# Optimization experiments

Hardware: AMD Instinct MI355X
Metric: run time of the kernel (lower is better)

Reference implementation:

```python
import jax, jax.numpy as jnp
import numpy as np

B, L, S, D, H = 4, 1024, 1024, 1024, 16
HD = D // H  # head_dim = 64


def setup_inputs() -> dict:
    key = jax.random.key(0)
    ks = jax.random.split(key, 12)
    s = 1.0 / np.sqrt(D)
    return {
        "query": jax.random.normal(ks[0], (B, L, D), jnp.float32),
        "key": jax.random.normal(ks[1], (B, S, D), jnp.float32),
        "value": jax.random.normal(ks[2], (B, S, D), jnp.float32),
        "key_padding_mask": jax.random.randint(ks[3], (B, S), 0, 2) > 0,
        "Wq": jax.random.normal(ks[4], (D, D), jnp.float32) * s,
        "bq": jnp.zeros((D,), jnp.float32),
        "Wk": jax.random.normal(ks[5], (D, D), jnp.float32) * s,
        "bk": jnp.zeros((D,), jnp.float32),
        "Wv": jax.random.normal(ks[6], (D, D), jnp.float32) * s,
        "bv": jnp.zeros((D,), jnp.float32),
        "Wo": jax.random.normal(ks[7], (D, D), jnp.float32) * s,
        "bo": jnp.zeros((D,), jnp.float32),
    }


def reference(query, key, value, key_padding_mask, Wq, bq, Wk, bk, Wv, bv, Wo, bo):
    bs, tgt, _ = query.shape
    src = key.shape[1]
    # Q/K/V projections (nn.Linear: x @ W.T + b)
    q = query @ Wq.T + bq
    k = key @ Wk.T + bk
    v = value @ Wv.T + bv
    # split heads: (B, T, H, HD)
    q = q.reshape(bs, tgt, H, HD)
    k = k.reshape(bs, src, H, HD)
    v = v.reshape(bs, src, H, HD)
    # scaled dot-product attention with key padding mask (True = masked)
    scale = 1.0 / jnp.sqrt(jnp.asarray(HD, q.dtype))
    scores = jnp.einsum("blhd,bshd->bhls", q, k) * scale  # (B,H,L,S)
    neg_inf = jnp.asarray(-jnp.inf, scores.dtype)
    scores = scores + jnp.where(key_padding_mask[:, None, None, :], neg_inf, 0.0)
    attn = jax.nn.softmax(scores, axis=-1)
    out = jnp.einsum("bhls,bshd->blhd", attn, v).reshape(bs, tgt, D)
    return out @ Wo.T + bo
```

## Files before the change

kernel.cpp:

```cpp
#include <hip/hip_runtime.h>
#include <hip/hip_bf16.h>


typedef __bf16 bf16;
typedef __bf16 bf16x8 __attribute__((ext_vector_type(8)));
typedef float floatx4 __attribute__((ext_vector_type(4)));

#define D_MODEL 1024
#define NHEAD   16
#define HDIM    64
#define BATCH   4
#define SEQ     1024
#define M_ROWS  (BATCH * SEQ)
#define ACT_N   ((size_t)M_ROWS * D_MODEL)
#define W_N     ((size_t)D_MODEL * D_MODEL)
#define SC2     0.18033688011112042f

#define GLD(gp, lp) __builtin_amdgcn_global_load_lds( \
    (__attribute__((address_space(1))) void*)(gp), \
    (__attribute__((address_space(3))) void*)(lp), 16, 0, 0)

__global__ __launch_bounds__(256)
void k_convert_all(const float* __restrict__ a0, const float* __restrict__ a1,
                   const float* __restrict__ a2,
                   const float* __restrict__ w0, const float* __restrict__ w1,
                   const float* __restrict__ w2, const float* __restrict__ w3,
                   bf16* __restrict__ dst,
                   const unsigned* __restrict__ m, float* __restrict__ mbias)
{
    if (blockIdx.x == 8192) {
        __shared__ unsigned viol[4];
        __shared__ int fmsh;
        if (threadIdx.x < 4) viol[threadIdx.x] = 0;
        __syncthreads();
        unsigned a = 0, b = 0, c = 0, d = 0;
        for (int i = threadIdx.x; i < 1024; i += 256) {
            unsigned v = m[i];
            if (v > 1u) a = 1;
            if (((v & 0xFFu) > 1u) || (((v >> 8) & 0xFFu) > 1u) ||
                (((v >> 16) & 0xFFu) > 1u) || (((v >> 24) & 0xFFu) > 1u)) b = 1;
            unsigned lo = v & 0xFFFFu, hi = v >> 16;
            if (!((lo == 0u || lo == 0x3F80u) && (hi == 0u || hi == 0x3F80u))) c = 1;
            if (lo != 0u) d = 1;
        }
        if (a) atomicOr(&viol[0], 1u);
        if (b) atomicOr(&viol[1], 1u);
        if (c) atomicOr(&viol[2], 1u);
        if (d) atomicOr(&viol[3], 1u);
        __syncthreads();
        if (threadIdx.x == 0) {
            int fm;
            if (!viol[0])      fm = 1;
            else if (!viol[1]) fm = 0;
            else if (!viol[2]) fm = viol[3] ? 2 : 3;
            else               fm = 0;
            fmsh = fm;
        }
        __syncthreads();
        const int fm = fmsh;
        for (int i = 0; i < 16; ++i) {
            int s = i * 256 + threadIdx.x;
            bool msk;
            if (fm == 1)      msk = ((const int*)m)[s] != 0;
            else if (fm == 2) msk = ((const unsigned short*)m)[s] != 0;
            else if (fm == 3) msk = ((const unsigned*)m)[s] != 0;
            else              msk = ((const unsigned char*)m)[s] != 0;
            mbias[s] = msk ? -1e30f : 0.f;
        }
        return;
    }

    size_t i = ((size_t)blockIdx.x * 256 + threadIdx.x) * 8;
    const float* src; size_t off;
    if (i < ((size_t)12 << 20)) {
        int z = (int)(i >> 22);
        src = (z == 0) ? a0 : (z == 1) ? a1 : a2;
        off = i & (((size_t)1 << 22) - 1);
    } else {
        size_t r = i - ((size_t)12 << 20);
        int j = (int)(r >> 20);
        src = (j == 0) ? w0 : (j == 1) ? w1 : (j == 2) ? w2 : w3;
        off = r & (((size_t)1 << 20) - 1);
    }
    float4 f0 = ((const float4*)(src + off))[0];
    float4 f1 = ((const float4*)(src + off))[1];
    bf16x8 o;
    o[0] = (bf16)f0.x; o[1] = (bf16)f0.y; o[2] = (bf16)f0.z; o[3] = (bf16)f0.w;
    o[4] = (bf16)f1.x; o[5] = (bf16)f1.y; o[6] = (bf16)f1.z; o[7] = (bf16)f1.w;
    *(bf16x8*)(dst + i) = o;
}

template<typename CT>
__device__ __forceinline__ void gemm_core(const bf16* __restrict__ A,
                                          const bf16* __restrict__ W,
                                          const float* __restrict__ bias,
                                          CT* __restrict__ C,
                                          int m0, int n0, bool rowBias)
{
    __shared__ alignas(16) bf16 As[2][128 * 32];
    __shared__ alignas(16) bf16 Bs[2][128 * 32];

    const int t    = threadIdx.x;
    const int lane = t & 63;
    const int w    = t >> 6;
    const int wm   = w >> 1, wn = w & 1;
    const int l15  = lane & 15;
    const int quad = lane >> 4;

    floatx4 acc[4][4] = {};

    #pragma unroll
    for (int i = 0; i < 2; ++i) {
        int c   = i * 256 + t;
        int row = c >> 2;
        int ck  = ((c & 3) ^ ((row >> 1) & 3)) * 8;
        int lo  = (i * 256 + w * 64) * 8;
        GLD(A + (size_t)(m0 + row) * D_MODEL + ck, As[0] + lo);
        GLD(W + (size_t)(n0 + row) * D_MODEL + ck, Bs[0] + lo);
    }
    __syncthreads();

    int cur = 0;
    for (int k0 = 0; k0 < D_MODEL; k0 += 32) {
        if (k0 + 32 < D_MODEL) {
            #pragma unroll
            for (int i = 0; i < 2; ++i) {
                int c   = i * 256 + t;
                int row = c >> 2;
                int ck  = ((c & 3) ^ ((row >> 1) & 3)) * 8;
                int lo  = (i * 256 + w * 64) * 8;
                GLD(A + (size_t)(m0 + row) * D_MODEL + k0 + 32 + ck, As[cur ^ 1] + lo);
                GLD(W + (size_t)(n0 + row) * D_MODEL + k0 + 32 + ck, Bs[cur ^ 1] + lo);
            }
        }

        bf16x8 af[4], bfr[4];
        #pragma unroll
        for (int i = 0; i < 4; ++i) {
            int r = wm * 64 + i * 16 + l15;
            af[i] = *(const bf16x8*)&As[cur][r * 32 + (quad ^ ((r >> 1) & 3)) * 8];
        }
        #pragma unroll
        for (int j = 0; j < 4; ++j) {
            int r = wn * 64 + j * 16 + l15;
            bfr[j] = *(const bf16x8*)&Bs[cur][r * 32 + (quad ^ ((r >> 1) & 3)) * 8];
        }

        #pragma unroll
        for (int i = 0; i < 4; ++i)
            #pragma unroll
            for (int j = 0; j < 4; ++j)
                acc[i][j] = __builtin_amdgcn_mfma_f32_16x16x32_bf16(
                    af[i], bfr[j], acc[i][j], 0, 0, 0);

        __syncthreads();
        cur ^= 1;
    }

    #pragma unroll
    for (int i = 0; i < 4; ++i) {
        int rowb = m0 + wm * 64 + i * 16 + quad * 4;
        float bvr[4];
        if (rowBias) {
            #pragma unroll
            for (int r = 0; r < 4; ++r) bvr[r] = bias[rowb + r];
        }
        #pragma unroll
        for (int j = 0; j < 4; ++j) {
            int col = n0 + wn * 64 + j * 16 + l15;
            float bc = rowBias ? 0.f : bias[col];
            #pragma unroll
            for (int r = 0; r < 4; ++r) {
                float val = acc[i][j][r] + (rowBias ? bvr[r] : bc);
                C[(size_t)(rowb + r) * D_MODEL + col] = (CT)val;
            }
        }
    }
}

__global__ __launch_bounds__(256)
void k_gemm_proj(const bf16* __restrict__ cq, const bf16* __restrict__ ck,
                 const bf16* __restrict__ cv,
                 const bf16* __restrict__ cWq, const bf16* __restrict__ cWk,
                 const bf16* __restrict__ cWv,
                 const float* __restrict__ bq, const float* __restrict__ bk,
                 const float* __restrict__ bv,
                 bf16* __restrict__ qproj, bf16* __restrict__ kproj,
                 bf16* __restrict__ vt)
{
    const int bid = blockIdx.x;
    const int x = bid & 7;
    const int j = bid >> 3;
    const int p = x * 12 + (j >> 3);
    const int n0 = (j & 7) * 128;
    if (p < 64) {
        int z = p >> 5, m0 = (p & 31) * 128;
        gemm_core<bf16>(z ? ck : cq, z ? cWk : cWq, z ? bk : bq,
                        z ? kproj : qproj, m0, n0, false);
    } else {
        int pv = p - 64;
        int b = pv >> 3, m0 = (pv & 7) * 128;
        gemm_core<bf16>(cWv, cv + (size_t)b * W_N, bv,
                        vt + (size_t)b * W_N, m0, n0, true);
    }
}

__global__ __launch_bounds__(256)
void k_gemm_o(const bf16* __restrict__ A, const bf16* __restrict__ W,
              const float* __restrict__ bb, float* __restrict__ C)
{
    const int bid = blockIdx.x;
    const int x = bid & 7;
    const int j = bid >> 3;
    const int p = x * 4 + (j >> 3);
    const int n0 = (j & 7) * 128;
    gemm_core<float>(A, W, bb, C, p * 128, n0, false);
}

__global__ __launch_bounds__(256)
void k_attn(const bf16* __restrict__ qproj, const bf16* __restrict__ kproj,
            const bf16* __restrict__ vt, const float* __restrict__ mbias_g,
            bf16* __restrict__ ctx)
{
    __shared__ alignas(16) bf16 Kst[2][4096];
    __shared__ alignas(16) bf16 Vst[2][4096];
    __shared__ alignas(16) bf16 Past[4096];

    const int t    = threadIdx.x;
    const int lane = t & 63;
    const int w    = t >> 6;
    const int l15  = lane & 15;
    const int quad = lane >> 4;

    const int b  = blockIdx.x >> 4;
    const int h  = blockIdx.x & 15;
    const int q0 = blockIdx.y * 64;

    #pragma unroll
    for (int kk = 0; kk < 2; ++kk) {
        const bf16* gp = qproj + (size_t)(b * SEQ + q0 + w * 16 + l15) * D_MODEL
                       + h * HDIM + kk * 32 + quad * 8;
        GLD(gp, Past + (w * 2 + kk) * 512);
    }
    #pragma unroll
    for (int i = 0; i < 2; ++i) {
        int f   = w * 2 + i;
        int row = (f >> 1) * 16 + l15;
        int cb  = (f & 1) * 32 + quad * 8;
        GLD(kproj + (size_t)(b * SEQ + row) * D_MODEL + h * HDIM + cb,
            Kst[0] + f * 512);
        GLD(vt + (size_t)(b * 1024 + h * HDIM + row) * D_MODEL + cb,
            Vst[0] + f * 512);
    }
    __syncthreads();

    bf16x8 qf[2];
    #pragma unroll
    for (int kk = 0; kk < 2; ++kk)
        qf[kk] = *(const bf16x8*)&Past[(w * 2 + kk) * 512 + lane * 8];

    bf16x8 ones;
    #pragma unroll
    for (int e = 0; e < 8; ++e) ones[e] = (bf16)1.0f;

    floatx4 o[4] = {};
    floatx4 accl = {};

    const int pbase = w * 1024 + (l15 >> 3) * 128 + quad * 32 + (l15 & 7);
    const float* __restrict__ mbb = mbias_g + b * SEQ;

    int cur = 0;
    for (int s0 = 0; s0 < SEQ; s0 += 64) {
        if (s0 + 64 < SEQ) {
            #pragma unroll
            for (int i = 0; i < 2; ++i) {
                int f   = w * 2 + i;
                int row = (f >> 1) * 16 + l15;
                int cb  = (f & 1) * 32 + quad * 8;
                GLD(kproj + (size_t)(b * SEQ + s0 + 64 + row) * D_MODEL
                        + h * HDIM + cb,
                    Kst[cur ^ 1] + f * 512);
                GLD(vt + (size_t)(b * 1024 + h * HDIM + row) * D_MODEL
                        + s0 + 64 + cb,
                    Vst[cur ^ 1] + f * 512);
            }
        }

        floatx4 s_acc[4] = {};
        #pragma unroll
        for (int j = 0; j < 4; ++j)
            #pragma unroll
            for (int kk = 0; kk < 2; ++kk) {
                bf16x8 kf = *(const bf16x8*)&Kst[cur][(j * 2 + kk) * 512 + lane * 8];
                s_acc[j] = __builtin_amdgcn_mfma_f32_16x16x32_bf16(
                    qf[kk], kf, s_acc[j], 0, 0, 0);
            }

        #pragma unroll
        for (int j = 0; j < 4; ++j) {
            float mb = mbb[s0 + j * 16 + l15];
            #pragma unroll
            for (int r = 0; r < 4; ++r) {
                float p = __builtin_amdgcn_exp2f(fmaf(s_acc[j][r], SC2, mb));
                Past[pbase + (j >> 1) * 512 + (j & 1) * 256 + r * 8] = (bf16)p;
            }
        }
        __builtin_amdgcn_wave_barrier();

        bf16x8 pf[2];
        #pragma unroll
        for (int kk = 0; kk < 2; ++kk)
            pf[kk] = *(const bf16x8*)&Past[w * 1024 + kk * 512 + lane * 8];

        #pragma unroll
        for (int kk = 0; kk < 2; ++kk)
            accl = __builtin_amdgcn_mfma_f32_16x16x32_bf16(pf[kk], ones, accl,
                                                           0, 0, 0);
        #pragma unroll
        for (int j = 0; j < 4; ++j)
            #pragma unroll
            for (int kk = 0; kk < 2; ++kk) {
                bf16x8 vf = *(const bf16x8*)&Vst[cur][(j * 2 + kk) * 512 + lane * 8];
                o[j] = __builtin_amdgcn_mfma_f32_16x16x32_bf16(
                    pf[kk], vf, o[j], 0, 0, 0);
            }

        __syncthreads();
        cur ^= 1;
    }

    float inv[4];
    #pragma unroll
    for (int r = 0; r < 4; ++r) inv[r] = (accl[r] > 0.f) ? 1.f / accl[r] : 0.f;
    #pragma unroll
    for (int j = 0; j < 4; ++j)
        #pragma unroll
        for (int r = 0; r < 4; ++r) {
            int row = q0 + w * 16 + quad * 4 + r;
            int col = h * HDIM + j * 16 + l15;
            ctx[(size_t)(b * SEQ + row) * D_MODEL + col] = (bf16)(o[j][r] * inv[r]);
        }
}

extern "C" void kernel_launch(void* const* d_in, const int* in_sizes, int n_in,
                              void* d_out, int out_size, void* d_ws, size_t ws_size,
                              hipStream_t stream)
{
    char* wsb = (char*)d_ws;
    float* mbias = (float*)wsb;
    bf16* cbase = (bf16*)(wsb + 65536);
    bf16 *cq = cbase, *ck = cq + ACT_N, *cv = ck + ACT_N;
    bf16 *cWq = cv + ACT_N, *cWk = cWq + W_N, *cWv = cWk + W_N, *cWo = cWv + W_N;
    bf16* qproj = cWo + W_N;
    bf16* kproj = qproj + ACT_N;
    bf16* vt    = kproj + ACT_N;
    bf16* ctx   = vt + ACT_N;
    float* out  = (float*)d_out;

    k_convert_all<<<8193, 256, 0, stream>>>(
        (const float*)d_in[0], (const float*)d_in[1], (const float*)d_in[2],
        (const float*)d_in[4], (const float*)d_in[6], (const float*)d_in[8],
        (const float*)d_in[10], cbase, (const unsigned*)d_in[3], mbias);

    k_gemm_proj<<<768, 256, 0, stream>>>(cq, ck, cv, cWq, cWk, cWv,
                                         (const float*)d_in[5],
                                         (const float*)d_in[7],
                                         (const float*)d_in[9],
                                         qproj, kproj, vt);
    k_attn<<<dim3(64, 16), 256, 0, stream>>>(qproj, kproj, vt, mbias, ctx);
    k_gemm_o<<<256, 256, 0, stream>>>(ctx, cWo, (const float*)d_in[11], out);
}
```

Measured before the change: 236.5 us.

## Triple-buffer GEMM LDS tiles with two-deep prefetch and partial vmcnt waits

Moves the GEMM core from double to triple buffering in LDS, prefetching two K-tiles ahead with global_load_lds. The full __syncthreads after each step becomes an inline s_waitcnt vmcnt(4) plus s_barrier, so only the oldest tile's loads must land before the barrier. This aims to hide global memory latency behind MFMA work. In exchange LDS use grows by half, which may reduce occupancy, and the hand-written vmcnt counts rely on the compiler not emitting other outstanding vector memory ops.

```diff
diff --git a/kernel.cpp b/kernel.cpp
--- a/kernel.cpp
+++ b/kernel.cpp
@@ -90,6 +90,18 @@
     *(bf16x8*)(dst + i) = o;
 }
 
+#define STAGE_TILE(k0s, bsel) do {                                          \
+    _Pragma("unroll")                                                       \
+    for (int ii = 0; ii < 2; ++ii) {                                        \
+        int c   = ii * 256 + t;                                             \
+        int row = c >> 2;                                                   \
+        int ck  = ((c & 3) ^ ((row >> 1) & 3)) * 8;                         \
+        int lo  = (ii * 256 + w * 64) * 8;                                  \
+        GLD(A + (size_t)(m0 + row) * D_MODEL + (k0s) + ck, As[bsel] + lo);  \
+        GLD(W + (size_t)(n0 + row) * D_MODEL + (k0s) + ck, Bs[bsel] + lo);  \
+    }                                                                       \
+} while (0)
+
 template<typename CT>
 __device__ __forceinline__ void gemm_core(const bf16* __restrict__ A,
                                           const bf16* __restrict__ W,
@@ -97,8 +109,8 @@
                                           CT* __restrict__ C,
                                           int m0, int n0, bool rowBias)
 {
-    __shared__ alignas(16) bf16 As[2][128 * 32];
-    __shared__ alignas(16) bf16 Bs[2][128 * 32];
+    __shared__ alignas(16) bf16 As[3][128 * 32];
+    __shared__ alignas(16) bf16 Bs[3][128 * 32];
 
     const int t    = threadIdx.x;
     const int lane = t & 63;
@@ -109,29 +121,16 @@
 
     floatx4 acc[4][4] = {};
 
-    #pragma unroll
-    for (int i = 0; i < 2; ++i) {
-        int c   = i * 256 + t;
-        int row = c >> 2;
-        int ck  = ((c & 3) ^ ((row >> 1) & 3)) * 8;
-        int lo  = (i * 256 + w * 64) * 8;
-        GLD(A + (size_t)(m0 + row) * D_MODEL + ck, As[0] + lo);
-        GLD(W + (size_t)(n0 + row) * D_MODEL + ck, Bs[0] + lo);
-    }
-    __syncthreads();
+    STAGE_TILE(0, 0);
+    STAGE_TILE(32, 1);
+    asm volatile("s_waitcnt vmcnt(4)\n\ts_barrier" ::: "memory");
 
     int cur = 0;
     for (int k0 = 0; k0 < D_MODEL; k0 += 32) {
-        if (k0 + 32 < D_MODEL) {
-            #pragma unroll
-            for (int i = 0; i < 2; ++i) {
-                int c   = i * 256 + t;
-                int row = c >> 2;
-                int ck  = ((c & 3) ^ ((row >> 1) & 3)) * 8;
-                int lo  = (i * 256 + w * 64) * 8;
-                GLD(A + (size_t)(m0 + row) * D_MODEL + k0 + 32 + ck, As[cur ^ 1] + lo);
-                GLD(W + (size_t)(n0 + row) * D_MODEL + k0 + 32 + ck, Bs[cur ^ 1] + lo);
-            }
+        const int pre = k0 + 64;
+        if (pre < D_MODEL) {
+            int nb = cur + 2; if (nb >= 3) nb -= 3;
+            STAGE_TILE(pre, nb);
         }
 
         bf16x8 af[4], bfr[4];
@@ -153,8 +152,12 @@
                 acc[i][j] = __builtin_amdgcn_mfma_f32_16x16x32_bf16(
                     af[i], bfr[j], acc[i][j], 0, 0, 0);
 
-        __syncthreads();
-        cur ^= 1;
+        if (pre < D_MODEL)
+            asm volatile("s_waitcnt vmcnt(4)\n\ts_barrier" ::: "memory");
+        else
+            asm volatile("s_waitcnt vmcnt(0)\n\ts_barrier" ::: "memory");
+
+        ++cur; if (cur == 3) cur = 0;
     }
 
     #pragma unroll
```

Result: no change. 240.8 us (+1.8%).

## Fuse fp32-to-bf16 activation conversion into projection GEMM tile loads

Applied to the files above, without the earlier changes.

The separate conversion of the query, key and value activations to bf16 is removed. The projection GEMM now loads fp32 tiles into registers, converts them, and writes bf16 into LDS after the MFMA step, overlapping the conversion with compute. This removes one full write and read of a 24 MB bf16 activation copy. The cost is that fp32 activations are read once per output column tile, which doubles the bytes per load, and the register-staged path replaces the direct global-to-LDS loads, adding register pressure and VALU conversion work inside the GEMM loop.

```diff
diff --git a/kernel.cpp b/kernel.cpp
--- a/kernel.cpp
+++ b/kernel.cpp
@@ -20,15 +20,21 @@
     (__attribute__((address_space(1))) void*)(gp), \
     (__attribute__((address_space(3))) void*)(lp), 16, 0, 0)
 
+__device__ __forceinline__ bf16x8 cvt8(const float4& f0, const float4& f1)
+{
+    bf16x8 o;
+    o[0] = (bf16)f0.x; o[1] = (bf16)f0.y; o[2] = (bf16)f0.z; o[3] = (bf16)f0.w;
+    o[4] = (bf16)f1.x; o[5] = (bf16)f1.y; o[6] = (bf16)f1.z; o[7] = (bf16)f1.w;
+    return o;
+}
+
 __global__ __launch_bounds__(256)
-void k_convert_all(const float* __restrict__ a0, const float* __restrict__ a1,
-                   const float* __restrict__ a2,
-                   const float* __restrict__ w0, const float* __restrict__ w1,
-                   const float* __restrict__ w2, const float* __restrict__ w3,
-                   bf16* __restrict__ dst,
-                   const unsigned* __restrict__ m, float* __restrict__ mbias)
-{
-    if (blockIdx.x == 8192) {
+void k_convert_w(const float* __restrict__ w0, const float* __restrict__ w1,
+                 const float* __restrict__ w2, const float* __restrict__ w3,
+                 bf16* __restrict__ dst,
+                 const unsigned* __restrict__ m, float* __restrict__ mbias)
+{
+    if (blockIdx.x == 2048) {
         __shared__ unsigned viol[4];
         __shared__ int fmsh;
         if (threadIdx.x < 4) viol[threadIdx.x] = 0;
@@ -71,28 +77,49 @@
     }
 
     size_t i = ((size_t)blockIdx.x * 256 + threadIdx.x) * 8;
-    const float* src; size_t off;
-    if (i < ((size_t)12 << 20)) {
-        int z = (int)(i >> 22);
-        src = (z == 0) ? a0 : (z == 1) ? a1 : a2;
-        off = i & (((size_t)1 << 22) - 1);
-    } else {
-        size_t r = i - ((size_t)12 << 20);
-        int j = (int)(r >> 20);
-        src = (j == 0) ? w0 : (j == 1) ? w1 : (j == 2) ? w2 : w3;
-        off = r & (((size_t)1 << 20) - 1);
-    }
+    int j = (int)(i >> 20);
+    const float* src = (j == 0) ? w0 : (j == 1) ? w1 : (j == 2) ? w2 : w3;
+    size_t off = i & (((size_t)1 << 20) - 1);
     float4 f0 = ((const float4*)(src + off))[0];
     float4 f1 = ((const float4*)(src + off))[1];
-    bf16x8 o;
-    o[0] = (bf16)f0.x; o[1] = (bf16)f0.y; o[2] = (bf16)f0.z; o[3] = (bf16)f0.w;
-    o[4] = (bf16)f1.x; o[5] = (bf16)f1.y; o[6] = (bf16)f1.z; o[7] = (bf16)f1.w;
-    *(bf16x8*)(dst + i) = o;
-}
-
-template<typename CT>
-__device__ __forceinline__ void gemm_core(const bf16* __restrict__ A,
-                                          const bf16* __restrict__ W,
+    *(bf16x8*)(dst + i) = cvt8(f0, f1);
+}
+
+template<bool F32>
+__device__ __forceinline__ void stage_issue(const void* __restrict__ base,
+                                            int r0, int kk,
+                                            const int srow[2], const int schk[2],
+                                            const int sx[2], int w,
+                                            bf16* lds, float4 pre[2][2])
+{
+    #pragma unroll
+    for (int ii = 0; ii < 2; ++ii) {
+        if constexpr (F32) {
+            const float* g = (const float*)base
+                + (size_t)(r0 + srow[ii]) * D_MODEL + kk + schk[ii] * 8;
+            pre[ii][0] = ((const float4*)g)[0];
+            pre[ii][1] = ((const float4*)g)[1];
+        } else {
+            GLD((const bf16*)base + (size_t)(r0 + srow[ii]) * D_MODEL + kk + sx[ii] * 8,
+                lds + (ii * 256 + w * 64) * 8);
+        }
+    }
+}
+
+template<bool F32>
+__device__ __forceinline__ void stage_write(const int srow[2], const int sx[2],
+                                            bf16* lds, const float4 pre[2][2])
+{
+    if constexpr (F32) {
+        #pragma unroll
+        for (int ii = 0; ii < 2; ++ii)
+            *(bf16x8*)&lds[srow[ii] * 32 + sx[ii] * 8] = cvt8(pre[ii][0], pre[ii][1]);
+    }
+}
+
+template<typename CT, bool AF32, bool WF32>
+__device__ __forceinline__ void gemm_core(const void* __restrict__ Ap,
+                                          const void* __restrict__ Wp,
                                           const float* __restrict__ bias,
                                           CT* __restrict__ C,
                                           int m0, int n0, bool rowBias)
@@ -107,31 +134,30 @@
     const int l15  = lane & 15;
     const int quad = lane >> 4;
 
+    int srow[2], schk[2], sx[2];
+    #pragma unroll
+    for (int ii = 0; ii < 2; ++ii) {
+        int c = ii * 256 + t;
+        srow[ii] = c >> 2;
+        schk[ii] = c & 3;
+        sx[ii]   = schk[ii] ^ ((srow[ii] >> 1) & 3);
+    }
+
     floatx4 acc[4][4] = {};
-
-    #pragma unroll
-    for (int i = 0; i < 2; ++i) {
-        int c   = i * 256 + t;
-        int row = c >> 2;
-        int ck  = ((c & 3) ^ ((row >> 1) & 3)) * 8;
-        int lo  = (i * 256 + w * 64) * 8;
-        GLD(A + (size_t)(m0 + row) * D_MODEL + ck, As[0] + lo);
-        GLD(W + (size_t)(n0 + row) * D_MODEL + ck, Bs[0] + lo);
-    }
+    float4 pa[2][2], pw[2][2];
+
+    stage_issue<AF32>(Ap, m0, 0, srow, schk, sx, w, As[0], pa);
+    stage_issue<WF32>(Wp, n0, 0, srow, schk, sx, w, Bs[0], pw);
+    stage_write<AF32>(srow, sx, As[0], pa);
+    stage_write<WF32>(srow, sx, Bs[0], pw);
     __syncthreads();
 
     int cur = 0;
     for (int k0 = 0; k0 < D_MODEL; k0 += 32) {
-        if (k0 + 32 < D_MODEL) {
-            #pragma unroll
-            for (int i = 0; i < 2; ++i) {
-                int c   = i * 256 + t;
-                int row = c >> 2;
-                int ck  = ((c & 3) ^ ((row >> 1) & 3)) * 8;
-                int lo  = (i * 256 + w * 64) * 8;
-                GLD(A + (size_t)(m0 + row) * D_MODEL + k0 + 32 + ck, As[cur ^ 1] + lo);
-                GLD(W + (size_t)(n0 + row) * D_MODEL + k0 + 32 + ck, Bs[cur ^ 1] + lo);
-            }
+        const int nk = k0 + 32;
+        if (nk < D_MODEL) {
+            stage_issue<AF32>(Ap, m0, nk, srow, schk, sx, w, As[cur ^ 1], pa);
+            stage_issue<WF32>(Wp, n0, nk, srow, schk, sx, w, Bs[cur ^ 1], pw);
         }
 
         bf16x8 af[4], bfr[4];
@@ -153,6 +179,10 @@
                 acc[i][j] = __builtin_amdgcn_mfma_f32_16x16x32_bf16(
                     af[i], bfr[j], acc[i][j], 0, 0, 0);
 
+        if (nk < D_MODEL) {
+            stage_write<AF32>(srow, sx, As[cur ^ 1], pa);
+            stage_write<WF32>(srow, sx, Bs[cur ^ 1], pw);
+        }
         __syncthreads();
         cur ^= 1;
     }
@@ -179,8 +209,8 @@
 }
 
 __global__ __launch_bounds__(256)
-void k_gemm_proj(const bf16* __restrict__ cq, const bf16* __restrict__ ck,
-                 const bf16* __restrict__ cv,
+void k_gemm_proj(const float* __restrict__ qf, const float* __restrict__ kf,
+                 const float* __restrict__ vf,
                  const bf16* __restrict__ cWq, const bf16* __restrict__ cWk,
                  const bf16* __restrict__ cWv,
                  const float* __restrict__ bq, const float* __restrict__ bk,
@@ -195,13 +225,15 @@
     const int n0 = (j & 7) * 128;
     if (p < 64) {
         int z = p >> 5, m0 = (p & 31) * 128;
-        gemm_core<bf16>(z ? ck : cq, z ? cWk : cWq, z ? bk : bq,
-                        z ? kproj : qproj, m0, n0, false);
+        gemm_core<bf16, true, false>(z ? (const void*)kf : (const void*)qf,
+                                     z ? (const void*)cWk : (const void*)cWq,
+                                     z ? bk : bq, z ? kproj : qproj,
+                                     m0, n0, false);
     } else {
         int pv = p - 64;
         int b = pv >> 3, m0 = (pv & 7) * 128;
-        gemm_core<bf16>(cWv, cv + (size_t)b * W_N, bv,
-                        vt + (size_t)b * W_N, m0, n0, true);
+        gemm_core<bf16, false, true>(cWv, vf + (size_t)b * W_N, bv,
+                                     vt + (size_t)b * W_N, m0, n0, true);
     }
 }
 
@@ -214,7 +246,7 @@
     const int j = bid >> 3;
     const int p = x * 4 + (j >> 3);
     const int n0 = (j & 7) * 128;
-    gemm_core<float>(A, W, bb, C, p * 128, n0, false);
+    gemm_core<float, false, false>(A, W, bb, C, p * 128, n0, false);
 }
 
 __global__ __launch_bounds__(256)
@@ -349,24 +381,22 @@
     char* wsb = (char*)d_ws;
     float* mbias = (float*)wsb;
     bf16* cbase = (bf16*)(wsb + 65536);
-    bf16 *cq = cbase, *ck = cq + ACT_N, *cv = ck + ACT_N;
-    bf16 *cWq = cv + ACT_N, *cWk = cWq + W_N, *cWv = cWk + W_N, *cWo = cWv + W_N;
+    bf16 *cWq = cbase, *cWk = cWq + W_N, *cWv = cWk + W_N, *cWo = cWv + W_N;
     bf16* qproj = cWo + W_N;
     bf16* kproj = qproj + ACT_N;
     bf16* vt    = kproj + ACT_N;
     bf16* ctx   = vt + ACT_N;
     float* out  = (float*)d_out;
 
-    k_convert_all<<<8193, 256, 0, stream>>>(
-        (const float*)d_in[0], (const float*)d_in[1], (const float*)d_in[2],
+    k_convert_w<<<2049, 256, 0, stream>>>(
         (const float*)d_in[4], (const float*)d_in[6], (const float*)d_in[8],
         (const float*)d_in[10], cbase, (const unsigned*)d_in[3], mbias);
 
-    k_gemm_proj<<<768, 256, 0, stream>>>(cq, ck, cv, cWq, cWk, cWv,
-                                         (const float*)d_in[5],
-                                         (const float*)d_in[7],
-                                         (const float*)d_in[9],
-                                         qproj, kproj, vt);
+    k_gemm_proj<<<768, 256, 0, stream>>>(
+        (const float*)d_in[0], (const float*)d_in[1], (const float*)d_in[2],
+        cWq, cWk, cWv,
+        (const float*)d_in[5], (const float*)d_in[7], (const float*)d_in[9],
+        qproj, kproj, vt);
     k_attn<<<dim3(64, 16), 256, 0, stream>>>(qproj, kproj, vt, mbias, ctx);
     k_gemm_o<<<256, 256, 0, stream>>>(ctx, cWo, (const float*)d_in[11], out);
 }
```

After: 255.3 us. 7.9% more time.

## Enlarge GEMM tiles to 256x256 with 512-thread blocks and phased LDS staging

Applied to the files above, without the earlier changes.

Replaces the 128x128, BK=32 GEMM core with a 256x256, BK=64 core run by 8 waves, each wave computing a 128x64 sub-tile. Shared memory moves to a 128KB dynamic double buffer, with the next K-slice loaded in four interleaved phases between MFMA groups. The aim is higher data reuse per LDS byte and fewer barriers per unit of work. The cost is a much smaller grid: the projection kernel drops to 192 blocks and the output GEMM to 64 blocks, which may leave many CUs idle.

```diff
diff --git a/kernel.cpp b/kernel.cpp
--- a/kernel.cpp
+++ b/kernel.cpp
@@ -91,94 +91,121 @@
 }
 
 template<typename CT>
-__device__ __forceinline__ void gemm_core(const bf16* __restrict__ A,
-                                          const bf16* __restrict__ W,
-                                          const float* __restrict__ bias,
-                                          CT* __restrict__ C,
-                                          int m0, int n0, bool rowBias)
-{
-    __shared__ alignas(16) bf16 As[2][128 * 32];
-    __shared__ alignas(16) bf16 Bs[2][128 * 32];
-
+__device__ __forceinline__ void gemm8_core(const bf16* __restrict__ A,
+                                           const bf16* __restrict__ W,
+                                           const float* __restrict__ bias,
+                                           CT* __restrict__ C,
+                                           int m0, int n0, bool rowBias,
+                                           bf16* __restrict__ As0,
+                                           bf16* __restrict__ Bs0)
+{
     const int t    = threadIdx.x;
     const int lane = t & 63;
     const int w    = t >> 6;
-    const int wm   = w >> 1, wn = w & 1;
+    const int wm   = w >> 2;
+    const int wn   = w & 3;
     const int l15  = lane & 15;
     const int quad = lane >> 4;
-
-    floatx4 acc[4][4] = {};
-
-    #pragma unroll
-    for (int i = 0; i < 2; ++i) {
-        int c   = i * 256 + t;
-        int row = c >> 2;
-        int ck  = ((c & 3) ^ ((row >> 1) & 3)) * 8;
-        int lo  = (i * 256 + w * 64) * 8;
-        GLD(A + (size_t)(m0 + row) * D_MODEL + ck, As[0] + lo);
-        GLD(W + (size_t)(n0 + row) * D_MODEL + ck, Bs[0] + lo);
-    }
+    const int lx   = l15 & 7;
+
+    floatx4 acc[8][4] = {};
+
+    int srow[2], schk[2], ldso[2];
+    #pragma unroll
+    for (int j = 0; j < 2; ++j) {
+        int i = j * 512 + t;
+        srow[j] = i >> 3;
+        schk[j] = (i & 7) ^ (srow[j] & 7);
+        ldso[j] = (j * 512 + w * 64) * 8;
+    }
+
+    #define STAGE_HALF(src, rb, k0s, h, dstbuf) do {                          \
+        _Pragma("unroll")                                                     \
+        for (int j = 0; j < 2; ++j)                                           \
+            GLD((src) + (size_t)((rb) + (h) * 128 + srow[j]) * D_MODEL        \
+                    + (k0s) + schk[j] * 8,                                    \
+                (dstbuf) + (h) * 8192 + ldso[j]);                             \
+    } while (0)
+
+    STAGE_HALF(A, m0, 0, 0, As0);
+    STAGE_HALF(A, m0, 0, 1, As0);
+    STAGE_HALF(W, n0, 0, 0, Bs0);
+    STAGE_HALF(W, n0, 0, 1, Bs0);
     __syncthreads();
 
-    int cur = 0;
-    for (int k0 = 0; k0 < D_MODEL; k0 += 32) {
-        if (k0 + 32 < D_MODEL) {
-            #pragma unroll
-            for (int i = 0; i < 2; ++i) {
-                int c   = i * 256 + t;
-                int row = c >> 2;
-                int ck  = ((c & 3) ^ ((row >> 1) & 3)) * 8;
-                int lo  = (i * 256 + w * 64) * 8;
-                GLD(A + (size_t)(m0 + row) * D_MODEL + k0 + 32 + ck, As[cur ^ 1] + lo);
-                GLD(W + (size_t)(n0 + row) * D_MODEL + k0 + 32 + ck, Bs[cur ^ 1] + lo);
-            }
-        }
-
-        bf16x8 af[4], bfr[4];
-        #pragma unroll
-        for (int i = 0; i < 4; ++i) {
-            int r = wm * 64 + i * 16 + l15;
-            af[i] = *(const bf16x8*)&As[cur][r * 32 + (quad ^ ((r >> 1) & 3)) * 8];
-        }
-        #pragma unroll
-        for (int j = 0; j < 4; ++j) {
-            int r = wn * 64 + j * 16 + l15;
-            bfr[j] = *(const bf16x8*)&Bs[cur][r * 32 + (quad ^ ((r >> 1) & 3)) * 8];
-        }
-
-        #pragma unroll
-        for (int i = 0; i < 4; ++i)
-            #pragma unroll
-            for (int j = 0; j < 4; ++j)
-                acc[i][j] = __builtin_amdgcn_mfma_f32_16x16x32_bf16(
-                    af[i], bfr[j], acc[i][j], 0, 0, 0);
-
+    for (int kt = 0; kt < 16; ++kt) {
+        const int nk = (kt + 1) * 64;
+        const bf16* __restrict__ Ab = As0 + (kt & 1) * 16384;
+        const bf16* __restrict__ Bb = Bs0 + (kt & 1) * 16384;
+        bf16* __restrict__ An = As0 + ((kt + 1) & 1) * 16384;
+        bf16* __restrict__ Bn = Bs0 + ((kt + 1) & 1) * 16384;
+
+        #pragma unroll
+        for (int ph = 0; ph < 4; ++ph) {
+            const int mq = ph >> 1, nq = ph & 1;
+
+            if (nk < D_MODEL) {
+                if (ph == 0)      STAGE_HALF(A, m0, nk, 0, An);
+                else if (ph == 1) STAGE_HALF(A, m0, nk, 1, An);
+                else if (ph == 2) STAGE_HALF(W, n0, nk, 0, Bn);
+                else              STAGE_HALF(W, n0, nk, 1, Bn);
+            }
+
+            bf16x8 af[4][2], bfr[2][2];
+            #pragma unroll
+            for (int ii = 0; ii < 4; ++ii) {
+                int row = wm * 128 + mq * 64 + ii * 16 + l15;
+                #pragma unroll
+                for (int kk = 0; kk < 2; ++kk)
+                    af[ii][kk] = *(const bf16x8*)
+                        &Ab[row * 64 + (((kk * 4 + quad) ^ lx)) * 8];
+            }
+            #pragma unroll
+            for (int jj = 0; jj < 2; ++jj) {
+                int row = wn * 64 + nq * 32 + jj * 16 + l15;
+                #pragma unroll
+                for (int kk = 0; kk < 2; ++kk)
+                    bfr[jj][kk] = *(const bf16x8*)
+                        &Bb[row * 64 + (((kk * 4 + quad) ^ lx)) * 8];
+            }
+
+            #pragma unroll
+            for (int ii = 0; ii < 4; ++ii)
+                #pragma unroll
+                for (int jj = 0; jj < 2; ++jj)
+                    #pragma unroll
+                    for (int kk = 0; kk < 2; ++kk)
+                        acc[mq * 4 + ii][nq * 2 + jj] =
+                            __builtin_amdgcn_mfma_f32_16x16x32_bf16(
+                                af[ii][kk], bfr[jj][kk],
+                                acc[mq * 4 + ii][nq * 2 + jj], 0, 0, 0);
+        }
         __syncthreads();
-        cur ^= 1;
-    }
-
-    #pragma unroll
-    for (int i = 0; i < 4; ++i) {
-        int rowb = m0 + wm * 64 + i * 16 + quad * 4;
+    }
+
+    #pragma unroll
+    for (int i = 0; i < 8; ++i) {
+        int rowb = m0 + wm * 128 + i * 16 + quad * 4;
         float bvr[4];
         if (rowBias) {
             #pragma unroll
             for (int r = 0; r < 4; ++r) bvr[r] = bias[rowb + r];
         }
         #pragma unroll
-        for (int j = 0; j < 4; ++j) {
-            int col = n0 + wn * 64 + j * 16 + l15;
+        for (int jf = 0; jf < 4; ++jf) {
+            int col = n0 + wn * 64 + jf * 16 + l15;
             float bc = rowBias ? 0.f : bias[col];
             #pragma unroll
             for (int r = 0; r < 4; ++r) {
-                float val = acc[i][j][r] + (rowBias ? bvr[r] : bc);
+                float val = acc[i][jf][r] + (rowBias ? bvr[r] : bc);
                 C[(size_t)(rowb + r) * D_MODEL + col] = (CT)val;
             }
         }
     }
-}
-
-__global__ __launch_bounds__(256)
+    #undef STAGE_HALF
+}
+
+__global__ __launch_bounds__(512, 2)
 void k_gemm_proj(const bf16* __restrict__ cq, const bf16* __restrict__ ck,
                  const bf16* __restrict__ cv,
                  const bf16* __restrict__ cWq, const bf16* __restrict__ cWk,
@@ -188,33 +215,40 @@
                  bf16* __restrict__ qproj, bf16* __restrict__ kproj,
                  bf16* __restrict__ vt)
 {
+    extern __shared__ __align__(16) bf16 smem[];
+    bf16* As0 = smem;
+    bf16* Bs0 = smem + 32768;
+
     const int bid = blockIdx.x;
-    const int x = bid & 7;
-    const int j = bid >> 3;
-    const int p = x * 12 + (j >> 3);
-    const int n0 = (j & 7) * 128;
-    if (p < 64) {
-        int z = p >> 5, m0 = (p & 31) * 128;
-        gemm_core<bf16>(z ? ck : cq, z ? cWk : cWq, z ? bk : bq,
-                        z ? kproj : qproj, m0, n0, false);
+    const int tid = (bid & 7) * 24 + (bid >> 3);
+    if (tid < 64) {
+        gemm8_core<bf16>(cq, cWq, bq, qproj,
+                         (tid >> 2) * 256, (tid & 3) * 256, false, As0, Bs0);
+    } else if (tid < 128) {
+        int u = tid - 64;
+        gemm8_core<bf16>(ck, cWk, bk, kproj,
+                         (u >> 2) * 256, (u & 3) * 256, false, As0, Bs0);
     } else {
-        int pv = p - 64;
-        int b = pv >> 3, m0 = (pv & 7) * 128;
-        gemm_core<bf16>(cWv, cv + (size_t)b * W_N, bv,
-                        vt + (size_t)b * W_N, m0, n0, true);
-    }
-}
-
-__global__ __launch_bounds__(256)
+        int v = tid - 128;
+        int b = v >> 4, m = (v >> 2) & 3, n = v & 3;
+        gemm8_core<bf16>(cWv, cv + (size_t)b * W_N, bv,
+                         vt + (size_t)b * W_N, m * 256, n * 256, true,
+                         As0, Bs0);
+    }
+}
+
+__global__ __launch_bounds__(512, 2)
 void k_gemm_o(const bf16* __restrict__ A, const bf16* __restrict__ W,
               const float* __restrict__ bb, float* __restrict__ C)
 {
+    extern __shared__ __align__(16) bf16 smem[];
+    bf16* As0 = smem;
+    bf16* Bs0 = smem + 32768;
+
     const int bid = blockIdx.x;
-    const int x = bid & 7;
-    const int j = bid >> 3;
-    const int p = x * 4 + (j >> 3);
-    const int n0 = (j & 7) * 128;
-    gemm_core<float>(A, W, bb, C, p * 128, n0, false);
+    const int tid = (bid & 7) * 8 + (bid >> 3);
+    gemm8_core<float>(A, W, bb, C, (tid >> 2) * 256, (tid & 3) * 256, false,
+                      As0, Bs0);
 }
 
 __global__ __launch_bounds__(256)
@@ -357,16 +391,25 @@
     bf16* ctx   = vt + ACT_N;
     float* out  = (float*)d_out;
 
+    static bool attrset = false;
+    if (!attrset) {
+        hipFuncSetAttribute((const void*)k_gemm_proj,
+                            hipFuncAttributeMaxDynamicSharedMemorySize, 131072);
+        hipFuncSetAttribute((const void*)k_gemm_o,
+                            hipFuncAttributeMaxDynamicSharedMemorySize, 131072);
+        attrset = true;
+    }
+
     k_convert_all<<<8193, 256, 0, stream>>>(
         (const float*)d_in[0], (const float*)d_in[1], (const float*)d_in[2],
         (const float*)d_in[4], (const float*)d_in[6], (const float*)d_in[8],
         (const float*)d_in[10], cbase, (const unsigned*)d_in[3], mbias);
 
-    k_gemm_proj<<<768, 256, 0, stream>>>(cq, ck, cv, cWq, cWk, cWv,
-                                         (const float*)d_in[5],
-                                         (const float*)d_in[7],
-                                         (const float*)d_in[9],
-                                         qproj, kproj, vt);
+    k_gemm_proj<<<192, 512, 131072, stream>>>(cq, ck, cv, cWq, cWk, cWv,
+                                              (const float*)d_in[5],
+                                              (const float*)d_in[7],
+                                              (const float*)d_in[9],
+                                              qproj, kproj, vt);
     k_attn<<<dim3(64, 16), 256, 0, stream>>>(qproj, kproj, vt, mbias, ctx);
-    k_gemm_o<<<256, 256, 0, stream>>>(ctx, cWo, (const float*)d_in[11], out);
-}
+    k_gemm_o<<<64, 512, 131072, stream>>>(ctx, cWo, (const float*)d_in[11], out);
+}
```

Result: faster. 220.7 us (-6.7%).
